# Kernel tuning notes

Hardware: AMD Instinct MI355X
Metric: run time of the kernel (lower is better)

The kernel has to match this reference:

```python
import jax, jax.numpy as jnp
import numpy as np

NUM_ANTENNAS = 16
D = 0.5
WAVELENGTH = 1.0
RHO = 0.8


def setup_inputs() -> dict:
    key = jax.random.key(0)
    k = jax.random.split(key, 5)
    return {
        "W": jax.random.normal(k[0], (2_000_000, 2 * NUM_ANTENNAS), dtype=jnp.float32),
        "Hc_real": jax.random.normal(k[1], (4, 8, NUM_ANTENNAS), dtype=jnp.float32),
        "Hc_imag": jax.random.normal(k[2], (4, 8, NUM_ANTENNAS), dtype=jnp.float32),
        "Hs_real": jax.random.normal(k[3], (4, 4, NUM_ANTENNAS), dtype=jnp.float32),
        "Hs_imag": jax.random.normal(k[4], (4, 4, NUM_ANTENNAS), dtype=jnp.float32),
    }


def _estimate_angles(h_real, h_imag):
    """Vectorized version of the per-(b,t) phase-unwrap + OLS slope fit.

    h_real/h_imag: [B, T, N] -> angles [B, T] in degrees.
    """
    n = jnp.arange(NUM_ANTENNAS, dtype=h_real.dtype)
    phases = jnp.arctan2(h_imag, h_real)                      # torch.angle
    pd = jnp.diff(phases, axis=-1)
    pd = (pd + jnp.pi) % (2.0 * jnp.pi) - jnp.pi              # wrap to (-pi, pi]
    zeros = jnp.zeros(phases.shape[:-1] + (1,), phases.dtype)
    unwrapped = jnp.concatenate([zeros, jnp.cumsum(pd, axis=-1)], axis=-1)  # [B,T,N]
    # OLS slope of unwrapped vs n (closed form of solve(XtX, XtY) with X=[n,1])
    n_c = n - n.mean()
    slope = (unwrapped * n_c).sum(-1) / (n_c * n_c).sum()     # [B,T]
    sin_theta = jnp.clip(slope * WAVELENGTH / (2.0 * jnp.pi * D), -1.0, 1.0)
    return -jnp.rad2deg(jnp.arcsin(sin_theta))


def _steering_phase(angles_deg):
    # phase[t, n] = 2*pi*d*n*sin(theta_t)/wavelength  -> [T, N]
    n = jnp.arange(NUM_ANTENNAS, dtype=angles_deg.dtype)
    s = jnp.sin(jnp.deg2rad(angles_deg))
    return 2.0 * jnp.pi * D * s[:, None] * n[None, :] / WAVELENGTH


def reference(W, Hc_real, Hc_imag, Hs_real, Hs_imag):
    user_angles = _estimate_angles(Hc_real, Hc_imag)[0]       # [Tc]
    target_angles = _estimate_angles(Hs_real, Hs_imag)[0]     # [Ts]

    Wr = W[:, :NUM_ANTENNAS]
    Wi = W[:, NUM_ANTENNAS:]

    def gains(phase):  # |w_cplx @ conj(sv).T|, all-real math
        c = jnp.cos(phase)  # [T, N]
        s = jnp.sin(phase)
        re = Wr @ c.T + Wi @ s.T  # [B, T]
        im = Wi @ c.T - Wr @ s.T
        return jnp.sqrt(re * re + im * im)

    user_gains = gains(_steering_phase(user_angles))          # [B, Tc]
    target_gains = gains(_steering_phase(target_angles))      # [B, Ts]

    min_user_gain = user_gains.min(axis=1)
    sum_user_gain = user_gains.sum(axis=1)
    avg_target_gain = target_gains.mean(axis=1)

    comm_loss = -RHO * 2.5 * (min_user_gain + 0.1 * sum_user_gain)
    sens_loss = -(1.0 - RHO) * avg_target_gain
    return jnp.mean(comm_loss + sens_loss)
```

## Files before the change

### kernel.cpp

```cpp
#include <hip/hip_runtime.h>
#include <math.h>

#define NA 16
#define NBEAM 12
#define NUSER 8

#define ACC_OFFSET 1536

__global__ void mtl_angles_kernel(const float* __restrict__ Hc_r, const float* __restrict__ Hc_i,
                                  const float* __restrict__ Hs_r, const float* __restrict__ Hs_i,
                                  float* __restrict__ table, double* __restrict__ acc) {
    int t = threadIdx.x;
    if (t == 0) *acc = 0.0;
    if (t >= NBEAM) return;

    const float* re;
    const float* im;
    if (t < NUSER) { re = Hc_r + t * NA;           im = Hc_i + t * NA; }
    else           { re = Hs_r + (t - NUSER) * NA; im = Hs_i + (t - NUSER) * NA; }

    const float PI_F   = 3.14159265358979323846f;
    const float TWO_PI = 6.28318530717958647692f;

    float ph[NA];
    #pragma unroll
    for (int n = 0; n < NA; ++n) ph[n] = atan2f(im[n], re[n]);

    float unw = 0.f, dotsum = 0.f;
    #pragma unroll
    for (int n = 1; n < NA; ++n) {
        float pd = ph[n] - ph[n - 1];
        float x  = pd + PI_F;
        float m  = fmodf(x, TWO_PI);
        if (m < 0.f) m += TWO_PI;
        pd = m - PI_F;
        unw += pd;
        dotsum += unw * ((float)n - 7.5f);
    }
    float slope = dotsum / 340.0f;
    float sin_theta = slope / PI_F;
    sin_theta = fminf(1.0f, fmaxf(-1.0f, sin_theta));
    float st = -sin_theta;

    #pragma unroll
    for (int n = 0; n < NA; ++n) {
        float phase = PI_F * st * (float)n;
        table[t * 2 * NA + n]      = cosf(phase);
        table[t * 2 * NA + NA + n] = sinf(phase);
    }
}

__device__ __forceinline__ float dot4(float4 a, float4 b) {
    return a.x * b.x + a.y * b.y + a.z * b.z + a.w * b.w;
}

__device__ __forceinline__ void load_lds16(const float* g, float* l) {
    __builtin_amdgcn_global_load_lds(
        (const __attribute__((address_space(1))) void*)g,
        (__attribute__((address_space(3))) void*)l, 16, 0, 0);
}

__device__ __forceinline__ float beam_gain(const float4* w, const float* trow) {
    const float4* tc = (const float4*)trow;
    float re = 0.f, im = 0.f;
    #pragma unroll
    for (int q = 0; q < 4; ++q) {
        float4 c = tc[q], s = tc[q + 4];
        float4 wr = w[q], wi = w[q + 4];
        re += dot4(wr, c) + dot4(wi, s);
        im += dot4(wi, c) - dot4(wr, s);
    }
    return sqrtf(re * re + im * im);
}

__device__ __forceinline__ float row_loss(const float4* w, const float* tbs) {
    float minU = 3.4e38f, sumU = 0.f, sumT = 0.f;
    #pragma unroll 1
    for (int j = 0; j < NBEAM; ++j) {
        float g = beam_gain(w, tbs + j * 32);
        if (j < NUSER) { minU = fminf(minU, g); sumU += g; }
        else           { sumT += g; }
    }
    return -2.0f * (minU + 0.1f * sumU) - 0.05f * sumT;
}

__global__ __launch_bounds__(256)
__attribute__((amdgpu_waves_per_eu(4, 4)))
void mtl_gains_kernel(const float* __restrict__ W,
                      const float* __restrict__ table,
                      double* __restrict__ acc, int rows) {
    __shared__ float sh[4 * 2 * 1024];
    __shared__ float tbs[NBEAM * 2 * NA];
    __shared__ float wsum[4];

    const int t = threadIdx.x;
    for (int i = t; i < NBEAM * 2 * NA; i += blockDim.x) tbs[i] = table[i];
    __syncthreads();

    const int wid  = t >> 6;
    const int lane = t & 63;
    float* buf0 = sh + wid * 2048;
    float* buf1 = buf0 + 1024;

    const int sq      = (lane & 7) ^ ((lane >> 3) & 7);
    const int src_off = (lane >> 3) * 32 + sq * 4;

    const int ntiles = rows >> 5;
    const int nwaves = gridDim.x * 4;
    const int gw     = blockIdx.x * 4 + wid;
    const int cnt    = ntiles / nwaves;
    const int rem    = ntiles % nwaves;
    const int t0     = gw * cnt + (gw < rem ? gw : rem);
    const int t1     = t0 + cnt + (gw < rem ? 1 : 0);

    const int h      = lane >> 5;
    const int row    = lane & 31;
    const float* tbU = tbs + h * 4 * 32;
    const float* tbT = tbs + (8 + h * 2) * 32;

    float local = 0.f;

    if (t0 < t1) {
        {
            const float* src = W + (size_t)t0 * 1024 + src_off;
            #pragma unroll
            for (int k = 0; k < 4; ++k) load_lds16(src + k * 256, buf0 + k * 256);
        }
        #pragma unroll 1
        for (int tt = t0; tt < t1; ++tt) {
            float* cur = ((tt - t0) & 1) ? buf1 : buf0;
            float* nxt = ((tt - t0) & 1) ? buf0 : buf1;
            if (tt + 1 < t1) {
                const float* src = W + (size_t)(tt + 1) * 1024 + src_off;
                #pragma unroll
                for (int k = 0; k < 4; ++k) load_lds16(src + k * 256, nxt + k * 256);
                asm volatile("s_waitcnt vmcnt(4)" ::: "memory");
            } else {
                asm volatile("s_waitcnt vmcnt(0)" ::: "memory");
            }

            const float* myrow = cur + row * 32;
            float4 w[8];
            #pragma unroll
            for (int q = 0; q < 8; ++q) {
                int s = q ^ (row & 7);
                w[q] = *(const float4*)(myrow + s * 4);
            }

            float minU = 3.4e38f, sumU = 0.f, sumT = 0.f;
            #pragma unroll 1
            for (int jj = 0; jj < 4; ++jj) {
                float g = beam_gain(w, tbU + jj * 32);
                minU = fminf(minU, g);
                sumU += g;
            }
            #pragma unroll 1
            for (int jj = 0; jj < 2; ++jj) {
                sumT += beam_gain(w, tbT + jj * 32);
            }
            minU = fminf(minU, __shfl_xor(minU, 32));
            sumU += __shfl_xor(sumU, 32);
            sumT += __shfl_xor(sumT, 32);
            local += 0.5f * (-2.0f * (minU + 0.1f * sumU) - 0.05f * sumT);
        }
    }

    int tailbase = ntiles << 5;
    if (blockIdx.x == 0) {
        int r = tailbase + t;
        if (r < rows) {
            const float4* wp = (const float4*)(W + (size_t)r * 32);
            float4 w[8];
            #pragma unroll
            for (int i = 0; i < 8; ++i) w[i] = wp[i];
            local += row_loss(w, tbs);
        }
    }

    #pragma unroll
    for (int off = 32; off > 0; off >>= 1) local += __shfl_down(local, off);
    if (lane == 0) wsum[wid] = local;
    __syncthreads();
    if (t == 0) {
        float b = wsum[0] + wsum[1] + wsum[2] + wsum[3];
        atomicAdd(acc, (double)b);
    }
}

__global__ void mtl_finalize_kernel(const double* __restrict__ acc, float* __restrict__ out, int rows) {
    if (threadIdx.x == 0) out[0] = (float)(*acc / (double)rows);
}

extern "C" void kernel_launch(void* const* d_in, const int* in_sizes, int n_in,
                              void* d_out, int out_size, void* d_ws, size_t ws_size,
                              hipStream_t stream) {
    const float* W    = (const float*)d_in[0];
    const float* Hc_r = (const float*)d_in[1];
    const float* Hc_i = (const float*)d_in[2];
    const float* Hs_r = (const float*)d_in[3];
    const float* Hs_i = (const float*)d_in[4];
    float* out = (float*)d_out;

    int rows = in_sizes[0] / (2 * NA);
    float*  table = (float*)d_ws;
    double* acc   = (double*)((char*)d_ws + ACC_OFFSET);

    mtl_angles_kernel<<<1, 64, 0, stream>>>(Hc_r, Hc_i, Hs_r, Hs_i, table, acc);

    mtl_gains_kernel<<<1024, 256, 0, stream>>>(W, table, acc, rows);

    mtl_finalize_kernel<<<1, 64, 0, stream>>>(acc, out, rows);
}
```

Before: 375.9 us.

## Process two rows per lane, reusing register-held steering vectors across them

Each wave now handles 64-row tiles, and each lane computes gains for two rows. Each steering-vector row is loaded from LDS into registers once and applied to both rows, halving the LDS table reads per row. The LDS staging buffers are doubled, occupancy is lowered to 2 waves per EU, and the grid is halved to 512 blocks. This trades latency hiding and parallelism for fewer LDS loads and more register-level reuse. The tail path now reads the table from global memory instead of LDS.

Measured after the change: 374.8 us. Within noise of the previous version (-0.3%).

```diff
diff --git a/kernel.cpp b/kernel.cpp
--- a/kernel.cpp
+++ b/kernel.cpp
@@ -60,12 +60,11 @@
         (__attribute__((address_space(3))) void*)l, 16, 0, 0);
 }
 
-__device__ __forceinline__ float beam_gain(const float4* w, const float* trow) {
-    const float4* tc = (const float4*)trow;
+__device__ __forceinline__ float beam_gain_reg(const float4* w, const float4 (&tb)[8]) {
     float re = 0.f, im = 0.f;
     #pragma unroll
     for (int q = 0; q < 4; ++q) {
-        float4 c = tc[q], s = tc[q + 4];
+        float4 c = tb[q], s = tb[q + 4];
         float4 wr = w[q], wi = w[q + 4];
         re += dot4(wr, c) + dot4(wi, s);
         im += dot4(wi, c) - dot4(wr, s);
@@ -73,11 +72,20 @@
     return sqrtf(re * re + im * im);
 }
 
-__device__ __forceinline__ float row_loss(const float4* w, const float* tbs) {
+__device__ __forceinline__ float row_loss(const float4* w, const float* tbl) {
     float minU = 3.4e38f, sumU = 0.f, sumT = 0.f;
     #pragma unroll 1
     for (int j = 0; j < NBEAM; ++j) {
-        float g = beam_gain(w, tbs + j * 32);
+        const float4* tc = (const float4*)(tbl + j * 32);
+        float re = 0.f, im = 0.f;
+        #pragma unroll
+        for (int q = 0; q < 4; ++q) {
+            float4 c = tc[q], s = tc[q + 4];
+            float4 wr = w[q], wi = w[q + 4];
+            re += dot4(wr, c) + dot4(wi, s);
+            im += dot4(wi, c) - dot4(wr, s);
+        }
+        float g = sqrtf(re * re + im * im);
         if (j < NUSER) { minU = fminf(minU, g); sumU += g; }
         else           { sumT += g; }
     }
@@ -85,11 +93,11 @@
 }
 
 __global__ __launch_bounds__(256)
-__attribute__((amdgpu_waves_per_eu(4, 4)))
+__attribute__((amdgpu_waves_per_eu(2, 2)))
 void mtl_gains_kernel(const float* __restrict__ W,
                       const float* __restrict__ table,
                       double* __restrict__ acc, int rows) {
-    __shared__ float sh[4 * 2 * 1024];
+    __shared__ float sh[4 * 2 * 2048];
     __shared__ float tbs[NBEAM * 2 * NA];
     __shared__ float wsum[4];
 
@@ -99,13 +107,18 @@
 
     const int wid  = t >> 6;
     const int lane = t & 63;
-    float* buf0 = sh + wid * 2048;
-    float* buf1 = buf0 + 1024;
+    float* buf0 = sh + wid * 4096;
+    float* buf1 = buf0 + 2048;
+
+    const int h      = lane >> 5;
+    const int row    = lane & 31;
+    const float* tbU = tbs + h * 4 * 32;
+    const float* tbT = tbs + (8 + h * 2) * 32;
 
     const int sq      = (lane & 7) ^ ((lane >> 3) & 7);
     const int src_off = (lane >> 3) * 32 + sq * 4;
 
-    const int ntiles = rows >> 5;
+    const int ntiles = rows >> 6;
     const int nwaves = gridDim.x * 4;
     const int gw     = blockIdx.x * 4 + wid;
     const int cnt    = ntiles / nwaves;
@@ -113,59 +126,71 @@
     const int t0     = gw * cnt + (gw < rem ? gw : rem);
     const int t1     = t0 + cnt + (gw < rem ? 1 : 0);
 
-    const int h      = lane >> 5;
-    const int row    = lane & 31;
-    const float* tbU = tbs + h * 4 * 32;
-    const float* tbT = tbs + (8 + h * 2) * 32;
-
     float local = 0.f;
 
     if (t0 < t1) {
         {
-            const float* src = W + (size_t)t0 * 1024 + src_off;
+            const float* src = W + (size_t)t0 * 2048 + src_off;
             #pragma unroll
-            for (int k = 0; k < 4; ++k) load_lds16(src + k * 256, buf0 + k * 256);
+            for (int k = 0; k < 8; ++k) load_lds16(src + k * 256, buf0 + k * 256);
         }
         #pragma unroll 1
         for (int tt = t0; tt < t1; ++tt) {
             float* cur = ((tt - t0) & 1) ? buf1 : buf0;
             float* nxt = ((tt - t0) & 1) ? buf0 : buf1;
             if (tt + 1 < t1) {
-                const float* src = W + (size_t)(tt + 1) * 1024 + src_off;
+                const float* src = W + (size_t)(tt + 1) * 2048 + src_off;
                 #pragma unroll
-                for (int k = 0; k < 4; ++k) load_lds16(src + k * 256, nxt + k * 256);
-                asm volatile("s_waitcnt vmcnt(4)" ::: "memory");
+                for (int k = 0; k < 8; ++k) load_lds16(src + k * 256, nxt + k * 256);
+                asm volatile("s_waitcnt vmcnt(8)" ::: "memory");
             } else {
                 asm volatile("s_waitcnt vmcnt(0)" ::: "memory");
             }
 
-            const float* myrow = cur + row * 32;
-            float4 w[8];
+            const float* r0 = cur + row * 32;
+            const float* r1 = cur + (row + 32) * 32;
+            float4 w0[8], w1[8];
             #pragma unroll
             for (int q = 0; q < 8; ++q) {
                 int s = q ^ (row & 7);
-                w[q] = *(const float4*)(myrow + s * 4);
-            }
-
-            float minU = 3.4e38f, sumU = 0.f, sumT = 0.f;
+                w0[q] = *(const float4*)(r0 + s * 4);
+                w1[q] = *(const float4*)(r1 + s * 4);
+            }
+
+            float minU0 = 3.4e38f, sumU0 = 0.f, sumT0 = 0.f;
+            float minU1 = 3.4e38f, sumU1 = 0.f, sumT1 = 0.f;
             #pragma unroll 1
             for (int jj = 0; jj < 4; ++jj) {
-                float g = beam_gain(w, tbU + jj * 32);
-                minU = fminf(minU, g);
-                sumU += g;
+                const float4* tc = (const float4*)(tbU + jj * 32);
+                float4 tb[8];
+                #pragma unroll
+                for (int q = 0; q < 8; ++q) tb[q] = tc[q];
+                float g0 = beam_gain_reg(w0, tb);
+                float g1 = beam_gain_reg(w1, tb);
+                minU0 = fminf(minU0, g0); sumU0 += g0;
+                minU1 = fminf(minU1, g1); sumU1 += g1;
             }
             #pragma unroll 1
             for (int jj = 0; jj < 2; ++jj) {
-                sumT += beam_gain(w, tbT + jj * 32);
-            }
-            minU = fminf(minU, __shfl_xor(minU, 32));
-            sumU += __shfl_xor(sumU, 32);
-            sumT += __shfl_xor(sumT, 32);
-            local += 0.5f * (-2.0f * (minU + 0.1f * sumU) - 0.05f * sumT);
-        }
-    }
-
-    int tailbase = ntiles << 5;
+                const float4* tc = (const float4*)(tbT + jj * 32);
+                float4 tb[8];
+                #pragma unroll
+                for (int q = 0; q < 8; ++q) tb[q] = tc[q];
+                sumT0 += beam_gain_reg(w0, tb);
+                sumT1 += beam_gain_reg(w1, tb);
+            }
+            minU0 = fminf(minU0, __shfl_xor(minU0, 32));
+            sumU0 += __shfl_xor(sumU0, 32);
+            sumT0 += __shfl_xor(sumT0, 32);
+            minU1 = fminf(minU1, __shfl_xor(minU1, 32));
+            sumU1 += __shfl_xor(sumU1, 32);
+            sumT1 += __shfl_xor(sumT1, 32);
+            local += 0.5f * (-2.0f * (minU0 + 0.1f * sumU0) - 0.05f * sumT0);
+            local += 0.5f * (-2.0f * (minU1 + 0.1f * sumU1) - 0.05f * sumT1);
+        }
+    }
+
+    int tailbase = ntiles << 6;
     if (blockIdx.x == 0) {
         int r = tailbase + t;
         if (r < rows) {
@@ -173,7 +198,7 @@
             float4 w[8];
             #pragma unroll
             for (int i = 0; i < 8; ++i) w[i] = wp[i];
-            local += row_loss(w, tbs);
+            local += row_loss(w, table);
         }
     }
 
@@ -207,7 +232,7 @@
 
     mtl_angles_kernel<<<1, 64, 0, stream>>>(Hc_r, Hc_i, Hs_r, Hs_i, table, acc);
 
-    mtl_gains_kernel<<<1024, 256, 0, stream>>>(W, table, acc, rows);
+    mtl_gains_kernel<<<512, 256, 0, stream>>>(W, table, acc, rows);
 
     mtl_finalize_kernel<<<1, 64, 0, stream>>>(acc, out, rows);
 }
```
